# Optimization experiments

Measured on AMD Instinct MI355X. Metric: run time of the kernel, lower is better.

The kernel has to match this reference:

```python
import jax, jax.numpy as jnp
import numpy as np

CUTOFFS = [2000, 10000, 50000]
HIDDEN = 1024
BATCH = 2048


def setup_inputs() -> dict:
    key = jax.random.key(0)
    ks = jax.random.split(key, 8)
    s = 1.0 / np.sqrt(HIDDEN)
    return {
        "hidden": jax.random.normal(ks[0], (BATCH, HIDDEN), dtype=jnp.float32),
        "target": jax.random.randint(ks[1], (BATCH,), 0, CUTOFFS[-1]),
        # head weight: candidates[:cutoffs[0]] plus 2 tail vectors, transposed -> (hidden, 2002)
        "head_w": jax.random.normal(ks[2], (HIDDEN, CUTOFFS[0] + 2), dtype=jnp.float32) * s,
        # tail 0 (cluster [2000,10000), size 8000): down 1024->1024 (rf^0), decode 1024->8000
        "down0": jax.random.normal(ks[3], (HIDDEN, HIDDEN), dtype=jnp.float32) * s,
        "dec0": jax.random.normal(ks[4], (HIDDEN, CUTOFFS[1] - CUTOFFS[0]), dtype=jnp.float32) * s,
        # tail 1 (cluster [10000,50000), size 40000): down 1024->256 (rf^1), decode 256->40000
        "down1": jax.random.normal(ks[5], (HIDDEN, HIDDEN // 4), dtype=jnp.float32) * s,
        "dec1": jax.random.normal(ks[6], (HIDDEN // 4, CUTOFFS[2] - CUTOFFS[1]), dtype=jnp.float32) * s,
    }


def reference(hidden, target, head_w, down0, dec0, down1, dec1):
    # Head logits over first bucket + one pseudo-token per tail cluster.
    head = hidden @ head_w  # (B, 2002)
    # Cluster membership masks (fixed shapes instead of data-dependent gather;
    # rows outside a cluster produce zeroed logits, matching index_select semantics
    # up to padding).
    m0 = ((target >= CUTOFFS[0]) & (target < CUTOFFS[1])).astype(hidden.dtype)
    m1 = ((target >= CUTOFFS[1]) & (target < CUTOFFS[2])).astype(hidden.dtype)
    # Grouped small matmuls: down-project then decode per tail cluster.
    t0 = ((hidden @ down0) @ dec0) * m0[:, None]  # (B, 8000)
    t1 = ((hidden @ down1) @ dec1) * m1[:, None]  # (B, 40000)
    return jnp.concatenate([head, t0, t1], axis=1)  # (B, 50002)
```

## Files before the change

kernel.cpp:

```cpp
#include <hip/hip_runtime.h>

typedef unsigned short u16;
typedef unsigned int   u32;
typedef __attribute__((ext_vector_type(4))) float  f32x4;
typedef __attribute__((ext_vector_type(8))) __bf16 bf16x8;
typedef __attribute__((ext_vector_type(8))) u16    u16x8;
typedef __attribute__((address_space(1))) void as1_void;
typedef __attribute__((address_space(3))) void as3_void;

__device__ __forceinline__ void async16(const void* g, void* l) {
  __builtin_amdgcn_global_load_lds((const as1_void*)g, (as3_void*)l, 16, 0, 0);
}

__device__ __forceinline__ u16 f2bf(float f) {
  u32 u = __builtin_bit_cast(u32, f);
  return (u16)((u + 0x7fffu + ((u >> 16) & 1u)) >> 16);
}

__global__ __launch_bounds__(256) void cvt_bf16_kernel(const float* __restrict__ in,
                                                       u16* __restrict__ out, int n8) {
  int i = blockIdx.x * 256 + threadIdx.x;
  if (i >= n8) return;
  const float4* p = reinterpret_cast<const float4*>(in) + (size_t)i * 2;
  float4 a = p[0], b = p[1];
  u16x8 o;
  o[0] = f2bf(a.x); o[1] = f2bf(a.y); o[2] = f2bf(a.z); o[3] = f2bf(a.w);
  o[4] = f2bf(b.x); o[5] = f2bf(b.y); o[6] = f2bf(b.z); o[7] = f2bf(b.w);
  reinterpret_cast<u16x8*>(out)[i] = o;
}

__global__ __launch_bounds__(256) void tconv_kernel(const float* __restrict__ in,
                                                    u16* __restrict__ out, int K, int N) {
  __shared__ float tile[32][33];
  int tx = threadIdx.x & 31, ty = threadIdx.x >> 5;
  int n0 = blockIdx.x * 32, k0 = blockIdx.y * 32;
#pragma unroll
  for (int i = 0; i < 4; i++) {
    int k = k0 + ty + i * 8;
    int n = n0 + tx;
    tile[ty + i * 8][tx] = (n < N) ? in[(size_t)k * N + n] : 0.0f;
  }
  __syncthreads();
#pragma unroll
  for (int i = 0; i < 4; i++) {
    int nn = n0 + ty + i * 8;
    out[(size_t)nn * K + k0 + tx] = f2bf(tile[tx][ty + i * 8]);
  }
}

template <bool STORE_BF16>
__global__ __launch_bounds__(256, 2)
void gemm_bt(const u16* __restrict__ A, const u16* __restrict__ Bt,
             void* __restrict__ Cout, int K, int ldc, int colOff, int Nreal,
             const int* __restrict__ target, int maskLo, int maskHi) {
  __shared__ u16 As[128 * 32];
  __shared__ u16 Bs[128 * 32];
  const int tid  = threadIdx.x;
  const int wid  = tid >> 6;
  const int lane = tid & 63;
  const int quad = lane >> 4;
  const int l16  = lane & 15;
  const int wm = (wid >> 1) * 64;
  const int wn = (wid & 1) * 64;
  const int bm = blockIdx.y * 128;
  const int bn = blockIdx.x * 128;

  f32x4 acc[4][4] = {};

  const int srow = wid * 16 + (lane >> 2);
  const int scol = (lane & 3) * 8;

  for (int k0 = 0; k0 < K; k0 += 32) {
    const u16* ga = A  + (size_t)(bm + srow) * K + k0 + scol;
    const u16* gb = Bt + (size_t)(bn + srow) * K + k0 + scol;
    async16(ga,                   As + wid * 512);
    async16(ga + (size_t)64 * K,  As + wid * 512 + 2048);
    async16(gb,                   Bs + wid * 512);
    async16(gb + (size_t)64 * K,  Bs + wid * 512 + 2048);
    __syncthreads();

    bf16x8 af[4], bfr[4];
#pragma unroll
    for (int i = 0; i < 4; i++) {
      af[i]  = *reinterpret_cast<const bf16x8*>(As + (wm + i * 16 + l16) * 32 + quad * 8);
      bfr[i] = *reinterpret_cast<const bf16x8*>(Bs + (wn + i * 16 + l16) * 32 + quad * 8);
    }
#pragma unroll
    for (int mi = 0; mi < 4; mi++)
#pragma unroll
      for (int ni = 0; ni < 4; ni++)
        acc[mi][ni] = __builtin_amdgcn_mfma_f32_16x16x32_bf16(af[mi], bfr[ni], acc[mi][ni], 0, 0, 0);
    __syncthreads();
  }

#pragma unroll
  for (int mi = 0; mi < 4; mi++) {
    const int rbase = bm + wm + mi * 16 + quad * 4;
    float msk[4];
#pragma unroll
    for (int r = 0; r < 4; r++) {
      if (!STORE_BF16 && maskLo >= 0) {
        int t = target[rbase + r];
        msk[r] = (t >= maskLo && t < maskHi) ? 1.0f : 0.0f;
      } else {
        msk[r] = 1.0f;
      }
    }
#pragma unroll
    for (int ni = 0; ni < 4; ni++) {
      const int col = bn + wn + ni * 16 + l16;
      if (STORE_BF16) {
        u16* C = (u16*)Cout;
#pragma unroll
        for (int r = 0; r < 4; r++)
          C[(size_t)(rbase + r) * ldc + col] = f2bf(acc[mi][ni][r]);
      } else if (col < Nreal) {
        float* C = (float*)Cout;
#pragma unroll
        for (int r = 0; r < 4; r++)
          C[(size_t)(rbase + r) * ldc + colOff + col] = acc[mi][ni][r] * msk[r];
      }
    }
  }
}

extern "C" void kernel_launch(void* const* d_in, const int* in_sizes, int n_in,
                              void* d_out, int out_size, void* d_ws, size_t ws_size,
                              hipStream_t stream) {
  const float* hidden = (const float*)d_in[0];
  const int*   target = (const int*)d_in[1];
  const float* head_w = (const float*)d_in[2];
  const float* down0  = (const float*)d_in[3];
  const float* dec0   = (const float*)d_in[4];
  const float* down1  = (const float*)d_in[5];
  const float* dec1   = (const float*)d_in[6];
  float* out = (float*)d_out;

  char* ws = (char*)d_ws;
  const size_t NEED = 53280768;
  if (ws_size < NEED) return;
  u16* hA      = (u16*)(ws);
  u16* head_wT = (u16*)(ws + 4194304);
  u16* down0T  = (u16*)(ws + 8388608);
  u16* dec0T   = (u16*)(ws + 10485760);
  u16* down1T  = (u16*)(ws + 27000832);
  u16* dec1T   = (u16*)(ws + 27525120);
  u16* X0      = (u16*)(ws + 48037888);
  u16* X1      = (u16*)(ws + 52232192);

  cvt_bf16_kernel<<<1024, 256, 0, stream>>>(hidden, hA, 262144);
  tconv_kernel<<<dim3(64, 32),  256, 0, stream>>>(head_w, head_wT, 1024, 2002);
  tconv_kernel<<<dim3(32, 32),  256, 0, stream>>>(down0,  down0T,  1024, 1024);
  tconv_kernel<<<dim3(252, 32), 256, 0, stream>>>(dec0,   dec0T,   1024, 8000);
  tconv_kernel<<<dim3(8, 32),   256, 0, stream>>>(down1,  down1T,  1024, 256);
  tconv_kernel<<<dim3(1252, 8), 256, 0, stream>>>(dec1,   dec1T,   256,  40000);

  const int LDC = 50002;
  gemm_bt<false><<<dim3(16, 16), 256, 0, stream>>>(hA, head_wT, out, 1024, LDC, 0, 2002,
                                                   nullptr, -1, 0);
  gemm_bt<true><<<dim3(8, 16), 256, 0, stream>>>(hA, down0T, X0, 1024, 1024, 0, 1024,
                                                 nullptr, -1, 0);
  gemm_bt<false><<<dim3(63, 16), 256, 0, stream>>>(X0, dec0T, out, 1024, LDC, 2002, 8000,
                                                   target, 2000, 10000);
  gemm_bt<true><<<dim3(2, 16), 256, 0, stream>>>(hA, down1T, X1, 1024, 256, 0, 256,
                                                 nullptr, -1, 0);
  gemm_bt<false><<<dim3(313, 16), 256, 0, stream>>>(X1, dec1T, out, 256, LDC, 10002, 40000,
                                                    target, 10000, 50000);
}
```

Before: 691.5 us.

## Compact tail-cluster rows by target and fuse launches into three kernels

Builds per-cluster index lists from target, then runs the down-projection and decode GEMMs only on the rows that belong to each cluster, gathering their inputs and scattering their outputs. Rows outside a cluster get zeros written directly instead of computed and masked. The eleven launches are merged into three (prep, first-stage GEMMs, second-stage GEMMs plus zero fill) to cut launch overhead. The prep kernel counts each cluster's rows with shared-memory atomics, so gather order is nondeterministic.

```diff
diff --git a/kernel.cpp b/kernel.cpp
--- a/kernel.cpp
+++ b/kernel.cpp
@@ -8,6 +8,10 @@
 typedef __attribute__((address_space(1))) void as1_void;
 typedef __attribute__((address_space(3))) void as3_void;
 
+__device__ int g_idx0[2048];
+__device__ int g_idx1[2048];
+__device__ int g_cnt[2];
+
 __device__ __forceinline__ void async16(const void* g, void* l) {
   __builtin_amdgcn_global_load_lds((const as1_void*)g, (as3_void*)l, 16, 0, 0);
 }
@@ -17,44 +21,13 @@
   return (u16)((u + 0x7fffu + ((u >> 16) & 1u)) >> 16);
 }
 
-__global__ __launch_bounds__(256) void cvt_bf16_kernel(const float* __restrict__ in,
-                                                       u16* __restrict__ out, int n8) {
-  int i = blockIdx.x * 256 + threadIdx.x;
-  if (i >= n8) return;
-  const float4* p = reinterpret_cast<const float4*>(in) + (size_t)i * 2;
-  float4 a = p[0], b = p[1];
-  u16x8 o;
-  o[0] = f2bf(a.x); o[1] = f2bf(a.y); o[2] = f2bf(a.z); o[3] = f2bf(a.w);
-  o[4] = f2bf(b.x); o[5] = f2bf(b.y); o[6] = f2bf(b.z); o[7] = f2bf(b.w);
-  reinterpret_cast<u16x8*>(out)[i] = o;
-}
-
-__global__ __launch_bounds__(256) void tconv_kernel(const float* __restrict__ in,
-                                                    u16* __restrict__ out, int K, int N) {
-  __shared__ float tile[32][33];
-  int tx = threadIdx.x & 31, ty = threadIdx.x >> 5;
-  int n0 = blockIdx.x * 32, k0 = blockIdx.y * 32;
-#pragma unroll
-  for (int i = 0; i < 4; i++) {
-    int k = k0 + ty + i * 8;
-    int n = n0 + tx;
-    tile[ty + i * 8][tx] = (n < N) ? in[(size_t)k * N + n] : 0.0f;
-  }
-  __syncthreads();
-#pragma unroll
-  for (int i = 0; i < 4; i++) {
-    int nn = n0 + ty + i * 8;
-    out[(size_t)nn * K + k0 + tx] = f2bf(tile[tx][ty + i * 8]);
-  }
-}
-
-template <bool STORE_BF16>
-__global__ __launch_bounds__(256, 2)
-void gemm_bt(const u16* __restrict__ A, const u16* __restrict__ Bt,
-             void* __restrict__ Cout, int K, int ldc, int colOff, int Nreal,
-             const int* __restrict__ target, int maskLo, int maskHi) {
-  __shared__ u16 As[128 * 32];
-  __shared__ u16 Bs[128 * 32];
+template <int MODE>
+__device__ __forceinline__ void gemm_core(
+    u16* As, u16* Bs,
+    const u16* __restrict__ A, const u16* __restrict__ Bt,
+    void* __restrict__ Cout, int K, int ldc, int colOff, int Nreal,
+    const int* __restrict__ idx, int cnt, int bm, int bn)
+{
   const int tid  = threadIdx.x;
   const int wid  = tid >> 6;
   const int lane = tid & 63;
@@ -62,21 +35,25 @@
   const int l16  = lane & 15;
   const int wm = (wid >> 1) * 64;
   const int wn = (wid & 1) * 64;
-  const int bm = blockIdx.y * 128;
-  const int bn = blockIdx.x * 128;
 
   f32x4 acc[4][4] = {};
 
   const int srow = wid * 16 + (lane >> 2);
   const int scol = (lane & 3) * 8;
 
+  size_t ar0, ar1;
+  if (MODE == 1) { ar0 = (size_t)idx[bm + srow]; ar1 = (size_t)idx[bm + srow + 64]; }
+  else           { ar0 = (size_t)(bm + srow);    ar1 = ar0 + 64; }
+  const u16* ga0 = A + ar0 * K + scol;
+  const u16* ga1 = A + ar1 * K + scol;
+  const u16* gb0 = Bt + (size_t)(bn + srow) * K + scol;
+  const u16* gb1 = gb0 + (size_t)64 * K;
+
   for (int k0 = 0; k0 < K; k0 += 32) {
-    const u16* ga = A  + (size_t)(bm + srow) * K + k0 + scol;
-    const u16* gb = Bt + (size_t)(bn + srow) * K + k0 + scol;
-    async16(ga,                   As + wid * 512);
-    async16(ga + (size_t)64 * K,  As + wid * 512 + 2048);
-    async16(gb,                   Bs + wid * 512);
-    async16(gb + (size_t)64 * K,  Bs + wid * 512 + 2048);
+    async16(ga0 + k0, As + wid * 512);
+    async16(ga1 + k0, As + wid * 512 + 2048);
+    async16(gb0 + k0, Bs + wid * 512);
+    async16(gb1 + k0, Bs + wid * 512 + 2048);
     __syncthreads();
 
     bf16x8 af[4], bfr[4];
@@ -96,31 +73,149 @@
 #pragma unroll
   for (int mi = 0; mi < 4; mi++) {
     const int rbase = bm + wm + mi * 16 + quad * 4;
-    float msk[4];
+    int  orow[4];
+    bool vld[4];
 #pragma unroll
     for (int r = 0; r < 4; r++) {
-      if (!STORE_BF16 && maskLo >= 0) {
-        int t = target[rbase + r];
-        msk[r] = (t >= maskLo && t < maskHi) ? 1.0f : 0.0f;
+      if (MODE == 2) {
+        int slot = rbase + r;
+        vld[r]  = slot < cnt;
+        orow[r] = vld[r] ? idx[slot] : 0;
       } else {
-        msk[r] = 1.0f;
+        vld[r] = true; orow[r] = rbase + r;
       }
     }
 #pragma unroll
     for (int ni = 0; ni < 4; ni++) {
       const int col = bn + wn + ni * 16 + l16;
-      if (STORE_BF16) {
+      if (MODE == 1) {
         u16* C = (u16*)Cout;
 #pragma unroll
         for (int r = 0; r < 4; r++)
-          C[(size_t)(rbase + r) * ldc + col] = f2bf(acc[mi][ni][r]);
-      } else if (col < Nreal) {
-        float* C = (float*)Cout;
-#pragma unroll
-        for (int r = 0; r < 4; r++)
-          C[(size_t)(rbase + r) * ldc + colOff + col] = acc[mi][ni][r] * msk[r];
+          C[(size_t)orow[r] * ldc + col] = f2bf(acc[mi][ni][r]);
+      } else {
+        if (col < Nreal) {
+          float* C = (float*)Cout;
+#pragma unroll
+          for (int r = 0; r < 4; r++)
+            if (vld[r]) C[(size_t)orow[r] * ldc + colOff + col] = acc[mi][ni][r];
+        }
       }
     }
+  }
+}
+
+__device__ __forceinline__ void tconv_core(float (*tile)[33], const float* __restrict__ in,
+                                           u16* __restrict__ out, int K, int N, int bx, int by) {
+  int tx = threadIdx.x & 31, ty = threadIdx.x >> 5;
+  int n0 = bx * 32, k0 = by * 32;
+#pragma unroll
+  for (int i = 0; i < 4; i++) {
+    int k = k0 + ty + i * 8;
+    int n = n0 + tx;
+    tile[ty + i * 8][tx] = (n < N) ? in[(size_t)k * N + n] : 0.0f;
+  }
+  __syncthreads();
+#pragma unroll
+  for (int i = 0; i < 4; i++)
+    out[(size_t)(n0 + ty + i * 8) * K + k0 + tx] = f2bf(tile[tx][ty + i * 8]);
+}
+
+__global__ __launch_bounds__(256) void prep(
+    const float* __restrict__ hidden, const int* __restrict__ target,
+    const float* __restrict__ head_w, const float* __restrict__ down0,
+    const float* __restrict__ dec0, const float* __restrict__ down1,
+    const float* __restrict__ dec1,
+    u16* __restrict__ hA, u16* __restrict__ head_wT, u16* __restrict__ down0T,
+    u16* __restrict__ dec0T, u16* __restrict__ down1T, u16* __restrict__ dec1T)
+{
+  __shared__ float tile[32][33];
+  __shared__ int cc[2];
+  const int b = blockIdx.x;
+  const int tid = threadIdx.x;
+  if (b < 1024) {
+    int i = b * 256 + tid;
+    const float4* p = reinterpret_cast<const float4*>(hidden) + (size_t)i * 2;
+    float4 a = p[0], c = p[1];
+    u16x8 o;
+    o[0] = f2bf(a.x); o[1] = f2bf(a.y); o[2] = f2bf(a.z); o[3] = f2bf(a.w);
+    o[4] = f2bf(c.x); o[5] = f2bf(c.y); o[6] = f2bf(c.z); o[7] = f2bf(c.w);
+    reinterpret_cast<u16x8*>(hA)[i] = o;
+  } else if (b < 3072) {
+    int r = b - 1024;  tconv_core(tile, head_w, head_wT, 1024, 2002,  r % 64,   r / 64);
+  } else if (b < 4096) {
+    int r = b - 3072;  tconv_core(tile, down0,  down0T,  1024, 1024,  r % 32,   r / 32);
+  } else if (b < 12160) {
+    int r = b - 4096;  tconv_core(tile, dec0,   dec0T,   1024, 8000,  r % 252,  r / 252);
+  } else if (b < 12416) {
+    int r = b - 12160; tconv_core(tile, down1,  down1T,  1024, 256,   r % 8,    r / 8);
+  } else if (b < 22432) {
+    int r = b - 12416; tconv_core(tile, dec1,   dec1T,   256,  40000, r % 1252, r / 1252);
+  } else {
+    if (tid < 2) cc[tid] = 0;
+    __syncthreads();
+    for (int i = tid; i < 2048; i += 256) {
+      int t = target[i];
+      if (t >= 2000 && t < 10000)  g_idx0[atomicAdd(&cc[0], 1)] = i;
+      else if (t >= 10000)         g_idx1[atomicAdd(&cc[1], 1)] = i;
+    }
+    __syncthreads();
+    int n0 = cc[0], n1 = cc[1];
+    for (int i = tid; i < 2048; i += 256) {
+      if (i >= n0) g_idx0[i] = 0;
+      if (i >= n1) g_idx1[i] = 0;
+    }
+    if (tid == 0) { g_cnt[0] = n0; g_cnt[1] = n1; }
+  }
+}
+
+__global__ __launch_bounds__(256, 2) void g1(
+    const u16* __restrict__ hA, const u16* __restrict__ head_wT,
+    const u16* __restrict__ down0T, const u16* __restrict__ down1T,
+    u16* __restrict__ X0c, u16* __restrict__ X1c, float* __restrict__ out)
+{
+  __shared__ u16 As[4096], Bs[4096];
+  const int b = blockIdx.x;
+  if (b < 256) {
+    gemm_core<0>(As, Bs, hA, head_wT, out, 1024, 50002, 0, 2002,
+                 nullptr, 2048, (b >> 4) * 128, (b & 15) * 128);
+  } else if (b < 384) {
+    int r = b - 256, bm = (r & 15) * 128, bn = (r >> 4) * 128;
+    if (bm < g_cnt[0])
+      gemm_core<1>(As, Bs, hA, down0T, X0c, 1024, 1024, 0, 1024, g_idx0, g_cnt[0], bm, bn);
+  } else {
+    int r = b - 384, bm = (r & 15) * 128, bn = (r >> 4) * 128;
+    if (bm < g_cnt[1])
+      gemm_core<1>(As, Bs, hA, down1T, X1c, 1024, 256, 0, 256, g_idx1, g_cnt[1], bm, bn);
+  }
+}
+
+__global__ __launch_bounds__(256, 2) void g2(
+    const u16* __restrict__ X0c, const u16* __restrict__ X1c,
+    const u16* __restrict__ dec0T, const u16* __restrict__ dec1T,
+    const int* __restrict__ target, float* __restrict__ out)
+{
+  __shared__ u16 As[4096], Bs[4096];
+  const int b = blockIdx.x;
+  if (b < 1008) {
+    int bm = (b & 15) * 128, bn = (b >> 4) * 128;
+    if (bm < g_cnt[0])
+      gemm_core<2>(As, Bs, X0c, dec0T, out, 1024, 50002, 2002, 8000, g_idx0, g_cnt[0], bm, bn);
+  } else if (b < 6016) {
+    int r = b - 1008, bm = (r & 15) * 128, bn = (r >> 4) * 128;
+    if (bm < g_cnt[1])
+      gemm_core<2>(As, Bs, X1c, dec1T, out, 256, 50002, 10002, 40000, g_idx1, g_cnt[1], bm, bn);
+  } else {
+    int row = b - 6016;
+    int t = target[row];
+    bool in0 = (t >= 2000) && (t < 10000);
+    bool in1 = (t >= 10000);
+    float2* p = reinterpret_cast<float2*>(out + (size_t)row * 50002);
+    float2 z; z.x = 0.0f; z.y = 0.0f;
+    if (!in0)
+      for (int i = threadIdx.x; i < 4000; i += 256)  p[1001 + i] = z;
+    if (!in1)
+      for (int i = threadIdx.x; i < 20000; i += 256) p[5001 + i] = z;
   }
 }
 
@@ -145,25 +240,11 @@
   u16* dec0T   = (u16*)(ws + 10485760);
   u16* down1T  = (u16*)(ws + 27000832);
   u16* dec1T   = (u16*)(ws + 27525120);
-  u16* X0      = (u16*)(ws + 48037888);
-  u16* X1      = (u16*)(ws + 52232192);
-
-  cvt_bf16_kernel<<<1024, 256, 0, stream>>>(hidden, hA, 262144);
-  tconv_kernel<<<dim3(64, 32),  256, 0, stream>>>(head_w, head_wT, 1024, 2002);
-  tconv_kernel<<<dim3(32, 32),  256, 0, stream>>>(down0,  down0T,  1024, 1024);
-  tconv_kernel<<<dim3(252, 32), 256, 0, stream>>>(dec0,   dec0T,   1024, 8000);
-  tconv_kernel<<<dim3(8, 32),   256, 0, stream>>>(down1,  down1T,  1024, 256);
-  tconv_kernel<<<dim3(1252, 8), 256, 0, stream>>>(dec1,   dec1T,   256,  40000);
-
-  const int LDC = 50002;
-  gemm_bt<false><<<dim3(16, 16), 256, 0, stream>>>(hA, head_wT, out, 1024, LDC, 0, 2002,
-                                                   nullptr, -1, 0);
-  gemm_bt<true><<<dim3(8, 16), 256, 0, stream>>>(hA, down0T, X0, 1024, 1024, 0, 1024,
-                                                 nullptr, -1, 0);
-  gemm_bt<false><<<dim3(63, 16), 256, 0, stream>>>(X0, dec0T, out, 1024, LDC, 2002, 8000,
-                                                   target, 2000, 10000);
-  gemm_bt<true><<<dim3(2, 16), 256, 0, stream>>>(hA, down1T, X1, 1024, 256, 0, 256,
-                                                 nullptr, -1, 0);
-  gemm_bt<false><<<dim3(313, 16), 256, 0, stream>>>(X1, dec1T, out, 256, LDC, 10002, 40000,
-                                                    target, 10000, 50000);
-}
+  u16* X0c     = (u16*)(ws + 48037888);
+  u16* X1c     = (u16*)(ws + 52232192);
+
+  prep<<<22433, 256, 0, stream>>>(hidden, target, head_w, down0, dec0, down1, dec1,
+                                  hA, head_wT, down0T, dec0T, down1T, dec1T);
+  g1<<<416, 256, 0, stream>>>(hA, head_wT, down0T, down1T, X0c, X1c, out);
+  g2<<<8064, 256, 0, stream>>>(X0c, X1c, dec0T, dec1T, target, out);
+}
```

New measurement: 603.9 us. 1.14x faster.
